# Optimization experiments

Measured on AMD Instinct MI355X. Metric: run time of the kernel, lower is better.

## Reference

```python
import jax, jax.numpy as jnp
import numpy as np

B, S, IN, OUT = 4, 8192, 768, 768
ALPHA = 0.01


def setup_inputs() -> dict:
    key = jax.random.key(0)
    kx, kw, kb = jax.random.split(key, 3)
    x = jax.random.randint(kx, (B, S, IN), -127, 127, dtype=jnp.int8)
    weight = jax.random.randint(kw, (IN, OUT), -127, 127, dtype=jnp.int8)
    bias = (jax.random.normal(kb, (1, OUT), dtype=jnp.float32) * 0.1).astype(jnp.float16)
    alpha = jnp.float32(ALPHA)
    return {"x": x, "weight": weight, "bias": bias, "alpha": alpha}


def reference(x, weight, bias, alpha):
    # x: [B, S, IN] int8, weight: [IN, OUT] int8 (Conv1D layout), bias: [1, OUT] fp16
    x_shape = x.shape
    xf = x.reshape(-1, x_shape[-1])                      # [N, IN] int8

    # rand_elements = zeros of x dtype (int8) -> masked_x == x, but keep the
    # wrap-bit detection chain faithful to the source.
    rand_elements = jnp.zeros_like(xf)                   # int8 zeros
    masked_x = xf + rand_elements                        # int8 wraparound add
    m32 = masked_x.astype(jnp.int32)
    x32 = xf.astype(jnp.int32)
    r32 = rand_elements.astype(jnp.int32)
    wraps = ((m32 ^ x32) & (m32 ^ r32) & 128) >> 7       # [N, IN] int32 (all zero here)
    wraps = jnp.where((wraps < 0) & (m32 < 0), 1, wraps)
    wraps = wraps.astype(jnp.int8)

    wf = weight.astype(jnp.float32)                      # [IN, OUT]
    # F.linear(masked_x.float(), weight.t().float()) == masked_x @ weight
    hidden = masked_x.astype(jnp.float32) @ wf           # [N, OUT] fp32
    overflow = ((wraps.astype(jnp.float32) @ wf).astype(jnp.int32) << 8)
    hidden = hidden + overflow.astype(jnp.float32)

    mask_mul = jnp.zeros((xf.shape[0], OUT), dtype=jnp.float32)
    y = hidden - mask_mul
    fp_y = y * alpha + bias.astype(jnp.float32)          # dequant scale + bias
    yq = jnp.clip(jnp.round(fp_y), -128, 127).astype(jnp.int8)
    return yq.reshape(*x_shape[:-1], -1)
```

## Files before the change

kernel.cpp:

```cpp
#include <hip/hip_runtime.h>

#define M_TOT 32768
#define K_TOT 768
#define N_TOT 768

typedef int v4i __attribute__((ext_vector_type(4)));

#define GLOAD_LDS(g, l) __builtin_amdgcn_global_load_lds( \
    (const __attribute__((address_space(1))) unsigned int*)(g), \
    (__attribute__((address_space(3))) unsigned int*)(l), 16, 0, 0)

__device__ __forceinline__ unsigned pack4(v4i a) {
  unsigned lo = __builtin_amdgcn_perm((unsigned)a.y, (unsigned)a.x, 0x00000400u);
  unsigned hi = __builtin_amdgcn_perm((unsigned)a.w, (unsigned)a.z, 0x00000400u);
  return __builtin_amdgcn_perm(hi, lo, 0x05040100u);
}

__global__ __launch_bounds__(256) void pack_w_kernel(const int* __restrict__ W,
                                                     signed char* __restrict__ W8T) {
  __shared__ signed char t[64][72];
  const int k0 = blockIdx.x * 64, n0 = blockIdx.y * 64;
  for (int i = threadIdx.x; i < 4096; i += 256) {
    int k = i >> 6, n = i & 63;
    t[n][k] = (signed char)W[(k0 + k) * N_TOT + n0 + n];
  }
  __syncthreads();
  for (int i = threadIdx.x; i < 4096; i += 256) {
    int n = i >> 6, k = i & 63;
    W8T[(n0 + n) * K_TOT + k0 + k] = t[n][k];
  }
}

__global__ __launch_bounds__(256, 4) void gemm_i8_kernel(
    const int* __restrict__ X, const signed char* __restrict__ W8T,
    const float* __restrict__ bias, const float* __restrict__ alpha_p,
    int* __restrict__ out) {
  __shared__ __align__(16) signed char Abuf[2][4096];
  __shared__ __align__(16) signed char Bbuf[2][8192];

  const int d = blockIdx.x;
  const int t = (d & 7) * 384 + (d >> 3);
  const int mt = t / 6, nt = t - mt * 6;
  const int row0 = mt << 6, col0 = nt << 7;

  const int tid = threadIdx.x;
  const int lane = tid & 63;
  const int wave = tid >> 6;
  const int wr = wave >> 1, wc = wave & 1;
  const int fr = lane & 15, fg = lane >> 4;
  const int fsw = (fr & 3) << 4;

  const int arow = tid >> 4;
  const int acol = (tid & 15) << 2;
  const int* Xbase = X + (row0 + arow) * K_TOT + acol;
  const int awsw = (arow & 3) << 4;

  int bsrc[2], bdst[2];
#pragma unroll
  for (int i = 0; i < 2; ++i) {
    int c = i * 256 + tid;
    int r = c >> 2, s = (c & 3) << 4;
    bsrc[i] = (col0 + r) * K_TOT + (s ^ ((r & 3) << 4));
    bdst[i] = i * 4096 + wave * 1024;
  }

  v4i q[2][4];
  const v4i zero = {0, 0, 0, 0};
  v4i acc[2][4];
#pragma unroll
  for (int m = 0; m < 2; ++m)
#pragma unroll
    for (int n = 0; n < 4; ++n) acc[m][n] = zero;

#define ISSUE_A(ks)                                                      \
  do {                                                                   \
    const int* _p = Xbase + (ks) * 64;                                   \
    _Pragma("unroll") for (int j = 0; j < 4; ++j)                        \
        q[(ks) & 1][j] = *(const v4i*)(_p + j * 16 * K_TOT);             \
  } while (0)

#define ISSUE_B(ks)                                                      \
  do {                                                                   \
    const signed char* _w = W8T + (ks) * 64;                             \
    signed char* _lb = Bbuf[(ks) & 1];                                   \
    GLOAD_LDS(_w + bsrc[0], _lb + bdst[0]);                              \
    GLOAD_LDS(_w + bsrc[1], _lb + bdst[1]);                              \
  } while (0)

#define PACK_WRITE_A(tt)                                                 \
  do {                                                                   \
    signed char* _ab = Abuf[(tt) & 1];                                   \
    _Pragma("unroll") for (int j = 0; j < 4; ++j) {                      \
      unsigned _dw = pack4(q[(tt) & 1][j]);                              \
      *(unsigned*)&_ab[(16 * j + arow) * 64 + (acol ^ awsw)] = _dw;      \
    }                                                                    \
  } while (0)

#define FRAGS_MFMA(ks)                                                   \
  do {                                                                   \
    v4i af[2], bf[4];                                                    \
    const signed char* _ab = Abuf[(ks) & 1];                             \
    const signed char* _bb = Bbuf[(ks) & 1];                             \
    const int _kb = (fg << 4) ^ fsw;                                     \
    _Pragma("unroll") for (int m = 0; m < 2; ++m)                        \
        af[m] = *(const v4i*)&_ab[(wr * 32 + m * 16 + fr) * 64 + _kb];   \
    _Pragma("unroll") for (int n = 0; n < 4; ++n)                        \
        bf[n] = *(const v4i*)&_bb[(wc * 64 + n * 16 + fr) * 64 + _kb];   \
    __builtin_amdgcn_s_setprio(1);                                       \
    _Pragma("unroll") for (int m = 0; m < 2; ++m)                        \
        _Pragma("unroll") for (int n = 0; n < 4; ++n)                    \
            acc[m][n] = __builtin_amdgcn_mfma_i32_16x16x64_i8(           \
                af[m], bf[n], acc[m][n], 0, 0, 0);                       \
    __builtin_amdgcn_s_setprio(0);                                       \
  } while (0)

#define GITER(ks, TOPW, MIDW)                                            \
  do {                                                                   \
    asm volatile("s_waitcnt vmcnt(" TOPW ") lgkmcnt(0)" ::: "memory");   \
    __builtin_amdgcn_s_barrier();                                        \
    if ((ks) + 1 < 12) ISSUE_B((ks) + 1);                                \
    if ((ks) + 2 < 12) ISSUE_A((ks) + 2);                                \
    FRAGS_MFMA(ks);                                                      \
    if ((ks) + 1 < 12) {                                                 \
      asm volatile("s_waitcnt vmcnt(" MIDW ")" ::: "memory");            \
      PACK_WRITE_A((ks) + 1);                                            \
    }                                                                    \
  } while (0)

  ISSUE_B(0); ISSUE_A(0); ISSUE_A(1);
  asm volatile("s_waitcnt vmcnt(4)" ::: "memory");
  PACK_WRITE_A(0);

  GITER(0, "4", "6");
  GITER(1, "4", "6");
  GITER(2, "4", "6");
  GITER(3, "4", "6");
  GITER(4, "4", "6");
  GITER(5, "4", "6");
  GITER(6, "4", "6");
  GITER(7, "4", "6");
  GITER(8, "4", "6");
  GITER(9, "4", "6");
  GITER(10, "4", "2");
  GITER(11, "0", "0");

  const float alpha = *alpha_p;
  float bv[4];
#pragma unroll
  for (int n = 0; n < 4; ++n) bv[n] = bias[col0 + wc * 64 + n * 16 + fr];

#pragma unroll
  for (int m = 0; m < 2; ++m) {
    int orow = row0 + wr * 32 + m * 16 + fg * 4;
#pragma unroll
    for (int n = 0; n < 4; ++n) {
      int ocol = col0 + wc * 64 + n * 16 + fr;
      int* po = out + orow * N_TOT + ocol;
#pragma unroll
      for (int r = 0; r < 4; ++r) {
        float v = rintf((float)acc[m][n][r] * alpha + bv[n]);
        v = fminf(127.f, fmaxf(-128.f, v));
        po[r * N_TOT] = (int)v;
      }
    }
  }
}

extern "C" void kernel_launch(void* const* d_in, const int* in_sizes, int n_in,
                              void* d_out, int out_size, void* d_ws, size_t ws_size,
                              hipStream_t stream) {
  const int* X = (const int*)d_in[0];
  const int* W = (const int*)d_in[1];
  const float* bias = (const float*)d_in[2];
  const float* alpha = (const float*)d_in[3];
  int* out = (int*)d_out;
  signed char* W8T = (signed char*)d_ws;

  dim3 pg(K_TOT / 64, N_TOT / 64);
  pack_w_kernel<<<pg, 256, 0, stream>>>(W, W8T);
  gemm_i8_kernel<<<(M_TOT / 64) * (N_TOT / 128), 256, 0, stream>>>(X, W8T, bias, alpha, out);
}
```

Measured before the change: 61.66 us.

## Grow GEMM block tile to 128x128 with 512 threads and reschedule A loads

The int8 GEMM block now covers 128 rows instead of 64 and runs 512 threads (8 waves), which halves the grid and doubles LDS for A. Each B tile fetched from global memory is reused across twice as many rows. The A prefetch now uses a single register set and is issued after the LDS write rather than two stages ahead. This shortens the prefetch distance, and the larger blocks plus extra LDS may lower occupancy.

```diff
diff --git a/kernel.cpp b/kernel.cpp
--- a/kernel.cpp
+++ b/kernel.cpp
@@ -31,17 +31,17 @@
   }
 }
 
-__global__ __launch_bounds__(256, 4) void gemm_i8_kernel(
+__global__ __launch_bounds__(512, 4) void gemm_i8_kernel(
     const int* __restrict__ X, const signed char* __restrict__ W8T,
     const float* __restrict__ bias, const float* __restrict__ alpha_p,
     int* __restrict__ out) {
-  __shared__ __align__(16) signed char Abuf[2][4096];
+  __shared__ __align__(16) signed char Abuf[2][8192];
   __shared__ __align__(16) signed char Bbuf[2][8192];
 
   const int d = blockIdx.x;
-  const int t = (d & 7) * 384 + (d >> 3);
+  const int t = (d & 7) * 192 + (d >> 3);
   const int mt = t / 6, nt = t - mt * 6;
-  const int row0 = mt << 6, col0 = nt << 7;
+  const int row0 = mt << 7, col0 = nt << 7;
 
   const int tid = threadIdx.x;
   const int lane = tid & 63;
@@ -55,16 +55,11 @@
   const int* Xbase = X + (row0 + arow) * K_TOT + acol;
   const int awsw = (arow & 3) << 4;
 
-  int bsrc[2], bdst[2];
-#pragma unroll
-  for (int i = 0; i < 2; ++i) {
-    int c = i * 256 + tid;
-    int r = c >> 2, s = (c & 3) << 4;
-    bsrc[i] = (col0 + r) * K_TOT + (s ^ ((r & 3) << 4));
-    bdst[i] = i * 4096 + wave * 1024;
-  }
+  const int bsrc = (col0 + (tid >> 2)) * K_TOT +
+                   (((tid & 3) << 4) ^ (((tid >> 2) & 3) << 4));
+  const int bdst = wave * 1024;
 
-  v4i q[2][4];
+  v4i q[4];
   const v4i zero = {0, 0, 0, 0};
   v4i acc[2][4];
 #pragma unroll
@@ -76,23 +71,18 @@
   do {                                                                   \
     const int* _p = Xbase + (ks) * 64;                                   \
     _Pragma("unroll") for (int j = 0; j < 4; ++j)                        \
-        q[(ks) & 1][j] = *(const v4i*)(_p + j * 16 * K_TOT);             \
+        q[j] = *(const v4i*)(_p + j * 32 * K_TOT);                       \
   } while (0)
 
 #define ISSUE_B(ks)                                                      \
-  do {                                                                   \
-    const signed char* _w = W8T + (ks) * 64;                             \
-    signed char* _lb = Bbuf[(ks) & 1];                                   \
-    GLOAD_LDS(_w + bsrc[0], _lb + bdst[0]);                              \
-    GLOAD_LDS(_w + bsrc[1], _lb + bdst[1]);                              \
-  } while (0)
+  GLOAD_LDS(W8T + (ks) * 64 + bsrc, &Bbuf[(ks) & 1][bdst])
 
 #define PACK_WRITE_A(tt)                                                 \
   do {                                                                   \
     signed char* _ab = Abuf[(tt) & 1];                                   \
     _Pragma("unroll") for (int j = 0; j < 4; ++j) {                      \
-      unsigned _dw = pack4(q[(tt) & 1][j]);                              \
-      *(unsigned*)&_ab[(16 * j + arow) * 64 + (acol ^ awsw)] = _dw;      \
+      unsigned _dw = pack4(q[j]);                                        \
+      *(unsigned*)&_ab[(32 * j + arow) * 64 + (acol ^ awsw)] = _dw;      \
     }                                                                    \
   } while (0)
 
@@ -114,35 +104,37 @@
     __builtin_amdgcn_s_setprio(0);                                       \
   } while (0)
 
-#define GITER(ks, TOPW, MIDW)                                            \
+#define GITER(ks, TOPW)                                                  \
   do {                                                                   \
     asm volatile("s_waitcnt vmcnt(" TOPW ") lgkmcnt(0)" ::: "memory");   \
     __builtin_amdgcn_s_barrier();                                        \
     if ((ks) + 1 < 12) ISSUE_B((ks) + 1);                                \
-    if ((ks) + 2 < 12) ISSUE_A((ks) + 2);                                \
     FRAGS_MFMA(ks);                                                      \
     if ((ks) + 1 < 12) {                                                 \
-      asm volatile("s_waitcnt vmcnt(" MIDW ")" ::: "memory");            \
+      asm volatile("s_waitcnt vmcnt(1)" ::: "memory");                   \
       PACK_WRITE_A((ks) + 1);                                            \
+      if ((ks) + 2 < 12) ISSUE_A((ks) + 2);                              \
     }                                                                    \
   } while (0)
 
-  ISSUE_B(0); ISSUE_A(0); ISSUE_A(1);
-  asm volatile("s_waitcnt vmcnt(4)" ::: "memory");
+  ISSUE_A(0);
+  ISSUE_B(0);
+  asm volatile("s_waitcnt vmcnt(1)" ::: "memory");
   PACK_WRITE_A(0);
+  ISSUE_A(1);
 
-  GITER(0, "4", "6");
-  GITER(1, "4", "6");
-  GITER(2, "4", "6");
-  GITER(3, "4", "6");
-  GITER(4, "4", "6");
-  GITER(5, "4", "6");
-  GITER(6, "4", "6");
-  GITER(7, "4", "6");
-  GITER(8, "4", "6");
-  GITER(9, "4", "6");
-  GITER(10, "4", "2");
-  GITER(11, "0", "0");
+  GITER(0, "4");
+  GITER(1, "4");
+  GITER(2, "4");
+  GITER(3, "4");
+  GITER(4, "4");
+  GITER(5, "4");
+  GITER(6, "4");
+  GITER(7, "4");
+  GITER(8, "4");
+  GITER(9, "4");
+  GITER(10, "4");
+  GITER(11, "0");
 
   const float alpha = *alpha_p;
   float bv[4];
@@ -178,5 +170,5 @@
 
   dim3 pg(K_TOT / 64, N_TOT / 64);
   pack_w_kernel<<<pg, 256, 0, stream>>>(W, W8T);
-  gemm_i8_kernel<<<(M_TOT / 64) * (N_TOT / 128), 256, 0, stream>>>(X, W8T, bias, alpha, out);
+  gemm_i8_kernel<<<(M_TOT / 128) * (N_TOT / 128), 512, 0, stream>>>(X, W8T, bias, alpha, out);
 }
```

Result: faster. 58.47 us (-5.2%).
